# Kernel tuning notes

Measured on AMD Instinct MI355X. Metric: run time of the kernel, lower is better.

The kernel has to match this reference:

```python
import jax, jax.numpy as jnp
import numpy as np
from jax import lax

B, L, T = 200000, 64, 16  # symbols, input length (== filter_size), channel taps


def _conv1d(x, w, stride):
    # x: [N, Cin, L], w: [Cout, Cin, K] -> [N, Cout, Lout]; lax conv = correlation (matches torch)
    return lax.conv_general_dilated(x, w, (stride,), 'VALID',
                                    dimension_numbers=('NCH', 'OIH', 'NCH'))


def setup_inputs() -> dict:
    key = jax.random.key(0)
    ks = jax.random.split(key, 7)
    return {
        'x': jax.random.normal(ks[0], (B, 2, L), dtype=jnp.float32),
        'conv1_w': jax.random.normal(ks[1], (1, 2, L // 4), dtype=jnp.float32) * 0.1,
        'conv1_b': jax.random.normal(ks[2], (1,), dtype=jnp.float32) * 0.1,
        'conv2_w': jax.random.normal(ks[3], (2, 1, 4), dtype=jnp.float32) * 0.1,
        'conv2_b': jax.random.normal(ks[4], (2,), dtype=jnp.float32) * 0.1,
        'taps_real': jax.random.normal(ks[5], (T,), dtype=jnp.float32),
        'taps_imag': jax.random.normal(ks[6], (T,), dtype=jnp.float32),
    }


def reference(x, conv1_w, conv1_b, conv2_w, conv2_b, taps_real, taps_imag):
    k1 = conv1_w.shape[2]  # filter_size // 4; stride == kernel
    h = jax.nn.elu(_conv1d(x, conv1_w, k1) + conv1_b[None, :, None])   # [B,1,4]
    rst = jax.nn.elu(_conv1d(h, conv2_w, 1) + conv2_b[None, :, None])  # [B,2,1]

    nT = taps_real.shape[0]
    sr = rst[:, 0, 0]  # real sequence over the batch/time axis, [B]
    si = rst[:, 1, 0]
    pr = jnp.pad(sr, (nT - 1, 0))  # causal zero padding, as torch.cat(zeros, rst)
    pi = jnp.pad(si, (nT - 1, 0))
    # torch code correlates windows with flipped taps -> use flipped taps as corr kernel
    hr = jnp.flip(taps_real)
    hi = jnp.flip(taps_imag)

    def corr(sig, ker):
        return lax.conv_general_dilated(sig[None, None, :], ker[None, None, :], (1,),
                                        'VALID', dimension_numbers=('NCH', 'OIH', 'NCH'))[0, 0]

    y_real = corr(pr, hr) - corr(pi, hi)  # [B]
    y_imag = corr(pr, hi) + corr(pi, hr)
    return jnp.stack([y_real, y_imag], axis=1)[:, :, None]  # [B,2,1]
```

## Files before the change

### kernel.cpp

```cpp
#include <hip/hip_runtime.h>
#include <math.h>

#define BLOCK 1024
#define EPB 256
#define TAPS 16
#define HWIN 16

__device__ __forceinline__ float eluf(float v) { return v > 0.f ? v : expm1f(v); }
__device__ __forceinline__ float dot4(float4 a, float4 b) {
    return a.x * b.x + a.y * b.y + a.z * b.z + a.w * b.w;
}

__device__ __forceinline__ void conv_elem(const float4* __restrict__ xf4, long ge,
        int j, float4 wv0, float4 wv1, float b1s,
        const float* __restrict__ w2, float b20, float b21,
        float& sr, float& si)
{
    const float4* base = xf4 + ge * 32;
    float4 v[8];
#pragma unroll
    for (int p = 0; p < 8; ++p) v[p] = base[4 * p + j];

    float a0 = 0.f, a1 = 0.f, a2 = 0.f, a3 = 0.f;
    a0 += dot4(v[0], wv0); a1 += dot4(v[1], wv0); a2 += dot4(v[2], wv0); a3 += dot4(v[3], wv0);
    a0 += dot4(v[4], wv1); a1 += dot4(v[5], wv1); a2 += dot4(v[6], wv1); a3 += dot4(v[7], wv1);

    a0 += __shfl_xor(a0, 1); a1 += __shfl_xor(a1, 1);
    a2 += __shfl_xor(a2, 1); a3 += __shfl_xor(a3, 1);
    a0 += __shfl_xor(a0, 2); a1 += __shfl_xor(a1, 2);
    a2 += __shfl_xor(a2, 2); a3 += __shfl_xor(a3, 2);

    float h0 = eluf(a0 + b1s), h1 = eluf(a1 + b1s);
    float h2 = eluf(a2 + b1s), h3 = eluf(a3 + b1s);

    float pr = b20 + h0 * w2[0] + h1 * w2[1] + h2 * w2[2] + h3 * w2[3];
    float pi = b21 + h0 * w2[4] + h1 * w2[5] + h2 * w2[6] + h3 * w2[7];
    sr = eluf(pr);
    si = eluf(pi);
}

__global__ __launch_bounds__(BLOCK, 4) void NF_20581483282566_kernel(
    const float* __restrict__ x,
    const float* __restrict__ w1, const float* __restrict__ b1,
    const float* __restrict__ w2, const float* __restrict__ b2,
    const float* __restrict__ tr, const float* __restrict__ ti,
    float2* __restrict__ out, int B)
{
    __shared__ float s_r[HWIN + EPB];
    __shared__ float s_i[HWIN + EPB];

    const int t = threadIdx.x;
    const int j = t & 3;
    const int e_loc = t >> 2;
    const long b0 = (long)blockIdx.x * EPB;
    const long ge = b0 + e_loc;

    const float4* xf4 = reinterpret_cast<const float4*>(x);
    const float4* w1v = reinterpret_cast<const float4*>(w1);
    const float4 wv0 = w1v[j];
    const float4 wv1 = w1v[4 + j];
    const float b1s = b1[0];
    const float b20 = b2[0], b21 = b2[1];

    if (ge < B) {
        float sr, si;
        conv_elem(xf4, ge, j, wv0, wv1, b1s, w2, b20, b21, sr, si);
        if (j == 0) { s_r[HWIN + e_loc] = sr; s_i[HWIN + e_loc] = si; }
    }

    if (t < 4 * HWIN) {
        const int eh = t >> 2;
        const long he = b0 - HWIN + eh;
        float sr = 0.f, si = 0.f;
        if (he >= 0)
            conv_elem(xf4, he, j, wv0, wv1, b1s, w2, b20, b21, sr, si);
        if (j == 0) { s_r[eh] = sr; s_i[eh] = si; }
    }
    __syncthreads();

    if (t < EPB) {
        const long b = b0 + t;
        if (b < B) {
            float yr = 0.f, yi = 0.f;
#pragma unroll
            for (int jj = 0; jj < TAPS; ++jj) {
                float a = s_r[HWIN + t - jj];
                float c = s_i[HWIN + t - jj];
                float trj = tr[jj], tij = ti[jj];
                yr += a * trj - c * tij;
                yi += a * tij + c * trj;
            }
            out[b] = make_float2(yr, yi);
        }
    }
}

extern "C" void kernel_launch(void* const* d_in, const int* in_sizes, int n_in,
                              void* d_out, int out_size, void* d_ws, size_t ws_size,
                              hipStream_t stream) {
    const float* x  = (const float*)d_in[0];
    const float* w1 = (const float*)d_in[1];
    const float* b1 = (const float*)d_in[2];
    const float* w2 = (const float*)d_in[3];
    const float* b2 = (const float*)d_in[4];
    const float* tr = (const float*)d_in[5];
    const float* ti = (const float*)d_in[6];
    float2* out = (float2*)d_out;

    const int B = in_sizes[0] / 128;
    const int grid = (B + EPB - 1) / EPB;
    NF_20581483282566_kernel<<<grid, BLOCK, 0, stream>>>(x, w1, b1, w2, b2, tr, ti, out, B);
}
```

Measured before the change: 24.03 us.

## Process multiple chunks per block with register prefetch of the next chunk

Switches to a fixed grid of 256 blocks. Each block walks a contiguous span of symbols in chunks of 256, prefetching the next chunk's inputs into registers while it computes the current one. The redundant 16-element halo recomputation now happens once per span instead of once per 256 elements, and the taps are cached in shared memory. The trade-off is fewer resident blocks per CU, which reduces the number of memory requests in flight. It also adds a block-wide barrier per chunk and leaves a partly filled final chunk in each span.

Result: slower. 25.63 us (+6.7%).

```diff
diff --git a/kernel.cpp b/kernel.cpp
--- a/kernel.cpp
+++ b/kernel.cpp
@@ -2,7 +2,8 @@
 #include <math.h>
 
 #define BLOCK 1024
-#define EPB 256
+#define CHUNK 256
+#define MAXCH 8
 #define TAPS 16
 #define HWIN 16
 
@@ -11,19 +12,15 @@
     return a.x * b.x + a.y * b.y + a.z * b.z + a.w * b.w;
 }
 
-__device__ __forceinline__ void conv_elem(const float4* __restrict__ xf4, long ge,
-        int j, float4 wv0, float4 wv1, float b1s,
+__device__ __forceinline__ void conv_from_regs(const float4* v,
+        float4 wv0, float4 wv1, float b1s,
         const float* __restrict__ w2, float b20, float b21,
         float& sr, float& si)
 {
-    const float4* base = xf4 + ge * 32;
-    float4 v[8];
-#pragma unroll
-    for (int p = 0; p < 8; ++p) v[p] = base[4 * p + j];
-
-    float a0 = 0.f, a1 = 0.f, a2 = 0.f, a3 = 0.f;
-    a0 += dot4(v[0], wv0); a1 += dot4(v[1], wv0); a2 += dot4(v[2], wv0); a3 += dot4(v[3], wv0);
-    a0 += dot4(v[4], wv1); a1 += dot4(v[5], wv1); a2 += dot4(v[6], wv1); a3 += dot4(v[7], wv1);
+    float a0 = dot4(v[0], wv0), a1 = dot4(v[1], wv0),
+          a2 = dot4(v[2], wv0), a3 = dot4(v[3], wv0);
+    a0 += dot4(v[4], wv1); a1 += dot4(v[5], wv1);
+    a2 += dot4(v[6], wv1); a3 += dot4(v[7], wv1);
 
     a0 += __shfl_xor(a0, 1); a1 += __shfl_xor(a1, 1);
     a2 += __shfl_xor(a2, 1); a3 += __shfl_xor(a3, 1);
@@ -33,10 +30,8 @@
     float h0 = eluf(a0 + b1s), h1 = eluf(a1 + b1s);
     float h2 = eluf(a2 + b1s), h3 = eluf(a3 + b1s);
 
-    float pr = b20 + h0 * w2[0] + h1 * w2[1] + h2 * w2[2] + h3 * w2[3];
-    float pi = b21 + h0 * w2[4] + h1 * w2[5] + h2 * w2[6] + h3 * w2[7];
-    sr = eluf(pr);
-    si = eluf(pi);
+    sr = eluf(b20 + h0 * w2[0] + h1 * w2[1] + h2 * w2[2] + h3 * w2[3]);
+    si = eluf(b21 + h0 * w2[4] + h1 * w2[5] + h2 * w2[6] + h3 * w2[7]);
 }
 
 __global__ __launch_bounds__(BLOCK, 4) void NF_20581483282566_kernel(
@@ -44,16 +39,20 @@
     const float* __restrict__ w1, const float* __restrict__ b1,
     const float* __restrict__ w2, const float* __restrict__ b2,
     const float* __restrict__ tr, const float* __restrict__ ti,
-    float2* __restrict__ out, int B)
+    float2* __restrict__ out, int B, int span)
 {
-    __shared__ float s_r[HWIN + EPB];
-    __shared__ float s_i[HWIN + EPB];
+    __shared__ float s_r[HWIN + MAXCH * CHUNK];
+    __shared__ float s_i[HWIN + MAXCH * CHUNK];
+    __shared__ float s_tr[TAPS], s_ti[TAPS];
 
-    const int t = threadIdx.x;
-    const int j = t & 3;
-    const int e_loc = t >> 2;
-    const long b0 = (long)blockIdx.x * EPB;
-    const long ge = b0 + e_loc;
+    const int t  = threadIdx.x;
+    const int j  = t & 3;
+    const int el = t >> 2;
+
+    const long span_start = (long)blockIdx.x * span;
+    const long span_end   = min(span_start + (long)span, (long)B);
+    if (span_start >= span_end) return;
+    const int nch = (int)((span_end - span_start + CHUNK - 1) / CHUNK);
 
     const float4* xf4 = reinterpret_cast<const float4*>(x);
     const float4* w1v = reinterpret_cast<const float4*>(w1);
@@ -62,36 +61,72 @@
     const float b1s = b1[0];
     const float b20 = b2[0], b21 = b2[1];
 
-    if (ge < B) {
-        float sr, si;
-        conv_elem(xf4, ge, j, wv0, wv1, b1s, w2, b20, b21, sr, si);
-        if (j == 0) { s_r[HWIN + e_loc] = sr; s_i[HWIN + e_loc] = si; }
+    float4 v[8];
+    bool own = (span_start + el) < span_end;
+    if (own) {
+        const float4* base = xf4 + (span_start + el) * 32;
+#pragma unroll
+        for (int p = 0; p < 8; ++p) v[p] = base[4 * p + j];
+    }
+    if (t < TAPS) { s_tr[t] = tr[t]; s_ti[t] = ti[t]; }
+
+    if (t < 60) {
+        const int  eh = t >> 2;
+        const long he = span_start - 15 + eh;
+        float sr = 0.f, si = 0.f;
+        if (he >= 0) {
+            float4 hv[8];
+            const float4* hbase = xf4 + he * 32;
+#pragma unroll
+            for (int p = 0; p < 8; ++p) hv[p] = hbase[4 * p + j];
+            conv_from_regs(hv, wv0, wv1, b1s, w2, b20, b21, sr, si);
+        }
+        if (j == 0) { s_r[1 + eh] = sr; s_i[1 + eh] = si; }
     }
 
-    if (t < 4 * HWIN) {
-        const int eh = t >> 2;
-        const long he = b0 - HWIN + eh;
-        float sr = 0.f, si = 0.f;
-        if (he >= 0)
-            conv_elem(xf4, he, j, wv0, wv1, b1s, w2, b20, b21, sr, si);
-        if (j == 0) { s_r[eh] = sr; s_i[eh] = si; }
-    }
-    __syncthreads();
+    for (int c = 0; c < nch; ++c) {
+        float4 vn[8];
+        bool own_n = false;
+        if (c + 1 < nch) {
+            const long gn = span_start + (long)(c + 1) * CHUNK + el;
+            own_n = gn < span_end;
+            if (own_n) {
+                const float4* nbase = xf4 + gn * 32;
+#pragma unroll
+                for (int p = 0; p < 8; ++p) vn[p] = nbase[4 * p + j];
+            }
+        }
 
-    if (t < EPB) {
-        const long b = b0 + t;
-        if (b < B) {
-            float yr = 0.f, yi = 0.f;
+        if (own) {
+            float sr, si;
+            conv_from_regs(v, wv0, wv1, b1s, w2, b20, b21, sr, si);
+            if (j == 0) {
+                s_r[HWIN + c * CHUNK + el] = sr;
+                s_i[HWIN + c * CHUNK + el] = si;
+            }
+        }
+        __syncthreads();
+
+        if (t < CHUNK) {
+            const long b = span_start + (long)c * CHUNK + t;
+            if (b < span_end) {
+                const int idx = HWIN + c * CHUNK + t;
+                float yr = 0.f, yi = 0.f;
 #pragma unroll
-            for (int jj = 0; jj < TAPS; ++jj) {
-                float a = s_r[HWIN + t - jj];
-                float c = s_i[HWIN + t - jj];
-                float trj = tr[jj], tij = ti[jj];
-                yr += a * trj - c * tij;
-                yi += a * tij + c * trj;
+                for (int jj = 0; jj < TAPS; ++jj) {
+                    float a = s_r[idx - jj];
+                    float cc = s_i[idx - jj];
+                    float trj = s_tr[jj], tij = s_ti[jj];
+                    yr += a * trj - cc * tij;
+                    yi += a * tij + cc * trj;
+                }
+                out[b] = make_float2(yr, yi);
             }
-            out[b] = make_float2(yr, yi);
         }
+
+#pragma unroll
+        for (int p = 0; p < 8; ++p) v[p] = vn[p];
+        own = own_n;
     }
 }
 
@@ -108,6 +143,8 @@
     float2* out = (float2*)d_out;
 
     const int B = in_sizes[0] / 128;
-    const int grid = (B + EPB - 1) / EPB;
-    NF_20581483282566_kernel<<<grid, BLOCK, 0, stream>>>(x, w1, b1, w2, b2, tr, ti, out, B);
+    const int grid = 256;
+    int span = (B + grid - 1) / grid;
+    NF_20581483282566_kernel<<<grid, BLOCK, 0, stream>>>(x, w1, b1, w2, b2, tr, ti,
+                                                         out, B, span);
 }
```
